# Performance work log

Hardware: AMD Instinct MI355X
Metric: run time of the kernel (lower is better)

Reference implementation:

```python
import jax, jax.numpy as jnp
import numpy as np

N = 50000
E = 800000
IN_CH = 256
OUT_CH = 64   # per-head channels (PyG out_channels)
HEADS = 4
NEG_SLOPE = 0.2


def setup_inputs() -> dict:
    key = jax.random.key(0)
    k = jax.random.split(key, 8)
    x = jax.random.normal(k[0], (N, IN_CH), dtype=jnp.float32)
    edge_index = jax.random.randint(k[1], (2, E), 0, N, dtype=jnp.int64)
    # GATConv parameters
    W = jax.random.normal(k[2], (IN_CH, HEADS * OUT_CH), dtype=jnp.float32) * (1.0 / np.sqrt(IN_CH))
    att_src = jax.random.normal(k[3], (HEADS, OUT_CH), dtype=jnp.float32) * 0.1
    att_dst = jax.random.normal(k[4], (HEADS, OUT_CH), dtype=jnp.float32) * 0.1
    bias = jnp.zeros((OUT_CH,), dtype=jnp.float32)
    # residual linear (bias=False)
    W_res = jax.random.normal(k[5], (IN_CH, OUT_CH), dtype=jnp.float32) * (1.0 / np.sqrt(IN_CH))
    return {"x": x, "edge_index": edge_index, "W": W, "att_src": att_src,
            "att_dst": att_dst, "bias": bias, "W_res": W_res}


def _gat_forward(x, edge_index, W, att_src, att_dst, bias, W_res):
    # residual branch
    x_res = x @ W_res                                   # [N, OUT_CH]

    # node transform: [N, H, C]
    xw = (x @ W).reshape(N, HEADS, OUT_CH)
    # per-node attention logits, [N, H]
    a_src = jnp.einsum('nhc,hc->nh', xw, att_src)
    a_dst = jnp.einsum('nhc,hc->nh', xw, att_dst)

    # add self-loops (PyG GATConv default add_self_loops=True)
    loops = jnp.arange(N, dtype=edge_index.dtype)
    src = jnp.concatenate([edge_index[0], loops])       # [E+N]
    dst = jnp.concatenate([edge_index[1], loops])       # [E+N]

    # per-edge logits + leaky relu, [E+N, H]
    alpha = jax.nn.leaky_relu(a_src[src] + a_dst[dst], NEG_SLOPE)

    # segment softmax over destination nodes
    m = jax.ops.segment_max(alpha, dst, num_segments=N)    # [N, H]
    e = jnp.exp(alpha - m[dst])
    denom = jax.ops.segment_sum(e, dst, num_segments=N)    # [N, H]
    a = e / denom[dst]                                     # [E+N, H]
    # (dropout p=0.1 on attention coeffs is identity in eval mode)

    # weighted scatter-aggregate: [N, H, C]
    msgs = xw[src] * a[:, :, None]
    out = jax.ops.segment_sum(msgs, dst, num_segments=N)

    # concat=False -> mean over heads, then bias
    x_conv = out.mean(axis=1) + bias                     # [N, OUT_CH]
    return jax.nn.relu(x_conv + x_res)


def reference(x, edge_index, W, att_src, att_dst, bias, W_res):
    return _gat_forward(x, edge_index, W, att_src, att_dst, bias, W_res)
```

## Files before the change

### kernel.cpp

```cpp
#include <hip/hip_runtime.h>
#include <math.h>

#define N_NODES 50000
#define N_EDGES 800000
#define IN_CH   256
#define OUT_CH  64
#define HEADS   4
#define NEG_SLOPE 0.2f
#define NCOLS   320
#define NTILES  20
#define NKK     8
#define PACK_BLOCKS 40
#define GEMM_BLOCKS 782
#define SCAN_BLOCKS 196
#define HIST_BLOCKS 3125
#define SCAT_BLOCKS 3125
#define AGG_BLOCKS  6250

typedef __attribute__((ext_vector_type(8))) short short8;
typedef __attribute__((ext_vector_type(4))) float f32x4;

__device__ __forceinline__ float lrelu(float v) {
    return v > 0.f ? v : NEG_SLOPE * v;
}
__device__ __forceinline__ unsigned bf16_rne(float f) {
    unsigned u = __float_as_uint(f);
    return (u + 0x7FFFu + ((u >> 16) & 1u)) >> 16;
}
__device__ __forceinline__ unsigned pack2(float lo, float hi) {
    return bf16_rne(lo) | (bf16_rne(hi) << 16);
}
__device__ __forceinline__ float bflo(unsigned u) { return __uint_as_float(u << 16); }
__device__ __forceinline__ float bfhi(unsigned u) { return __uint_as_float(u & 0xFFFF0000u); }
__device__ __forceinline__ short8 as_short8(uint4 u) {
    union { uint4 u4; short8 s8; } cv; cv.u4 = u; return cv.s8;
}

__global__ __launch_bounds__(256) void pack_B(
    const float* __restrict__ W, const float* __restrict__ Wres,
    uint4* __restrict__ Bp)
{
    const int idx  = blockIdx.x * 256 + threadIdx.x;
    const int kk   = idx / (NTILES * 64);
    const int rem  = idx - kk * (NTILES * 64);
    const int t    = rem >> 6;
    const int lane = rem & 63;
    const int colL = lane & 15, quad = lane >> 4;
    const int col  = t * 16 + colL;
    const int k0   = kk * 32 + quad * 8;
    float v[8];
    #pragma unroll
    for (int j = 0; j < 8; ++j) {
        const int k = k0 + j;
        v[j] = (col < IN_CH) ? W[(size_t)k * IN_CH + col]
                             : Wres[(size_t)k * OUT_CH + (col - IN_CH)];
    }
    uint4 u;
    u.x = pack2(v[0], v[1]); u.y = pack2(v[2], v[3]);
    u.z = pack2(v[4], v[5]); u.w = pack2(v[6], v[7]);
    Bp[(kk * NTILES + t) * 64 + lane] = u;
}

__global__ __launch_bounds__(256) void hist_gemm(
    const float* __restrict__ x, const uint4* __restrict__ Bp,
    uint2* __restrict__ xw2, float* __restrict__ xres,
    const int* __restrict__ ei, int* __restrict__ cnt,
    int* __restrict__ epos,
    const float* __restrict__ attS, const float* __restrict__ attD,
    float* __restrict__ asrc, float* __restrict__ adst)
{
    __shared__ uint4 Alds[4 * NKK * 64];
    __shared__ float logS[64][HEADS];
    __shared__ float logD[64][HEADS];

    if (blockIdx.x >= GEMM_BLOCKS) {
        const int e = (blockIdx.x - GEMM_BLOCKS) * 256 + threadIdx.x;
        if (e < N_EDGES)
            epos[e] = atomicAdd(&cnt[ei[N_EDGES + e]], 1);
        return;
    }

    const int tid = threadIdx.x;
    const int n0  = blockIdx.x * 64;

    logS[tid >> 2][tid & 3] = 0.f;
    logD[tid >> 2][tid & 3] = 0.f;

    #pragma unroll
    for (int i = 0; i < 8; ++i) {
        const int e    = i * 256 + tid;
        const int g    = e >> 9;
        const int kk   = (e >> 6) & 7;
        const int lane = e & 63;
        const int cL   = lane & 15, qd = lane >> 4;
        const int row  = n0 + g * 16 + cL;
        const int k0   = kk * 32 + qd * 8;
        uint4 u = make_uint4(0u, 0u, 0u, 0u);
        if (row < N_NODES) {
            const float4 a = *reinterpret_cast<const float4*>(x + (size_t)row * IN_CH + k0);
            const float4 b = *reinterpret_cast<const float4*>(x + (size_t)row * IN_CH + k0 + 4);
            u.x = pack2(a.x, a.y); u.y = pack2(a.z, a.w);
            u.z = pack2(b.x, b.y); u.w = pack2(b.z, b.w);
        }
        Alds[(g * NKK + kk) * 64 + lane] = u;
    }
    __syncthreads();

    const int lane = tid & 63;
    const int wv   = tid >> 6;
    const int colL = lane & 15, quad = lane >> 4;

    f32x4 acc[4][5];
    #pragma unroll
    for (int rg = 0; rg < 4; ++rg)
        #pragma unroll
        for (int j = 0; j < 5; ++j) acc[rg][j] = (f32x4){0.f, 0.f, 0.f, 0.f};

    for (int kk = 0; kk < NKK; ++kk) {
        uint4 bu[5];
        #pragma unroll
        for (int j = 0; j < 5; ++j)
            bu[j] = Bp[(kk * NTILES + j * 4 + wv) * 64 + lane];
        #pragma unroll
        for (int rg = 0; rg < 4; ++rg) {
            const short8 a = as_short8(Alds[(rg * NKK + kk) * 64 + lane]);
            #pragma unroll
            for (int j = 0; j < 5; ++j)
                acc[rg][j] = __builtin_amdgcn_mfma_f32_16x16x32_bf16(
                    a, as_short8(bu[j]), acc[rg][j], 0, 0, 0);
        }
    }

    #pragma unroll
    for (int rg = 0; rg < 4; ++rg) {
        #pragma unroll
        for (int r = 0; r < 4; ++r) {
            const int row = n0 + rg * 16 + quad * 4 + r;
            if (row < N_NODES) {
                xw2[(size_t)row * 64 + wv * 16 + colL] = make_uint2(
                    pack2(acc[rg][0][r], acc[rg][1][r]),
                    pack2(acc[rg][2][r], acc[rg][3][r]));
                xres[(size_t)row * OUT_CH + wv * 16 + colL] = acc[rg][4][r];
            }
        }
    }

    float aSr[HEADS], aDr[HEADS];
    #pragma unroll
    for (int h = 0; h < HEADS; ++h) {
        aSr[h] = attS[h * 64 + wv * 16 + colL];
        aDr[h] = attD[h * 64 + wv * 16 + colL];
    }
    #pragma unroll
    for (int rg = 0; rg < 4; ++rg) {
        #pragma unroll
        for (int h = 0; h < HEADS; ++h) {
            #pragma unroll
            for (int r = 0; r < 4; ++r) {
                float vS = acc[rg][h][r] * aSr[h];
                float vD = acc[rg][h][r] * aDr[h];
                #pragma unroll
                for (int m = 1; m < 16; m <<= 1) {
                    vS += __shfl_xor(vS, m);
                    vD += __shfl_xor(vD, m);
                }
                if (colL == 0) {
                    atomicAdd(&logS[rg * 16 + quad * 4 + r][h], vS);
                    atomicAdd(&logD[rg * 16 + quad * 4 + r][h], vD);
                }
            }
        }
    }
    __syncthreads();
    {
        const int rl = tid >> 2, h = tid & 3;
        const int row = n0 + rl;
        if (row < N_NODES) {
            asrc[(size_t)row * HEADS + h] = logS[rl][h];
            adst[(size_t)row * HEADS + h] = logD[rl][h];
        }
    }
}

__global__ __launch_bounds__(256) void scan_local(
    const int* __restrict__ cnt, int* __restrict__ lscan, int* __restrict__ bsum)
{
    __shared__ int ws[4];
    const int t = threadIdx.x, lane = t & 63, w = t >> 6;
    const int i = blockIdx.x * 256 + t;
    const int v = (i < N_NODES) ? cnt[i] : 0;
    int sc = v;
    #pragma unroll
    for (int off = 1; off < 64; off <<= 1) {
        const int n = __shfl_up(sc, off);
        if (lane >= off) sc += n;
    }
    if (lane == 63) ws[w] = sc;
    __syncthreads();
    int prefix = 0;
    for (int j = 0; j < w; ++j) prefix += ws[j];
    if (i < N_NODES) lscan[i] = prefix + sc - v;
    if (t == 255) bsum[blockIdx.x] = prefix + sc;
}

__global__ __launch_bounds__(256) void scatter_edges(
    const int* __restrict__ ei, const int* __restrict__ epos,
    const int* __restrict__ lscan, const int* __restrict__ bsum,
    int* __restrict__ esrc)
{
    __shared__ int bsx[256];
    __shared__ int ws[4];
    const int t = threadIdx.x;
    const int lane = t & 63, wv = t >> 6;

    const int v = (t < SCAN_BLOCKS) ? bsum[t] : 0;
    int sc = v;
    #pragma unroll
    for (int off = 1; off < 64; off <<= 1) {
        const int n = __shfl_up(sc, off);
        if (lane >= off) sc += n;
    }
    if (lane == 63) ws[wv] = sc;
    __syncthreads();
    int prefix = 0;
    for (int j = 0; j < wv; ++j) prefix += ws[j];
    bsx[t] = prefix + sc - v;
    __syncthreads();

    const int e = blockIdx.x * 256 + t;
    if (e < N_EDGES) {
        const int d = ei[N_EDGES + e];
        esrc[lscan[d] + bsx[d >> 8] + epos[e]] = ei[e];
    }
}

__global__ __launch_bounds__(256) void aggregate(
    const int* __restrict__ esrc, const int* __restrict__ lscan,
    const int* __restrict__ bsum, const int* __restrict__ cnt,
    const float* __restrict__ asrc, const float* __restrict__ adst,
    const uint2* __restrict__ xw2, const float* __restrict__ xres,
    const float* __restrict__ bias, float* __restrict__ out,
    const int d0)
{
    __shared__ float4 wbuf[4][64];
    __shared__ int    sbuf[4][64];
    __shared__ int    bsx[256];
    __shared__ int    ws[4];
    const int t = threadIdx.x;
    const int lane = t & 63;
    const int wv   = t >> 6;

    {
        const int v = (t < SCAN_BLOCKS) ? bsum[t] : 0;
        int sc = v;
        #pragma unroll
        for (int off = 1; off < 64; off <<= 1) {
            const int n = __shfl_up(sc, off);
            if (lane >= off) sc += n;
        }
        if (lane == 63) ws[wv] = sc;
        __syncthreads();
        int prefix = 0;
        for (int j = 0; j < wv; ++j) prefix += ws[j];
        bsx[t] = prefix + sc - v;
        __syncthreads();
    }

    const int d = d0 + blockIdx.x * 4 + wv;
    const int row = lscan[d] + bsx[d >> 8];
    const int deg = cnt[d];
    const float4 ad = *reinterpret_cast<const float4*>(adst + (size_t)d * 4);
    const char* xwB = (const char*)xw2;
    const int laneB = lane << 3;

    float dn0 = 0.f, dn1 = 0.f, dn2 = 0.f, dn3 = 0.f;
    float ac0 = 0.f, ac1 = 0.f, ac2 = 0.f, ac3 = 0.f;

    for (int base = 0; base < deg; base += 64) {
        const int m = min(64, deg - base);
        if (lane < m) {
            const int s = esrc[row + base + lane];
            const float4 as = *reinterpret_cast<const float4*>(asrc + (size_t)s * 4);
            const float e0 = __expf(lrelu(as.x + ad.x));
            const float e1 = __expf(lrelu(as.y + ad.y));
            const float e2 = __expf(lrelu(as.z + ad.z));
            const float e3 = __expf(lrelu(as.w + ad.w));
            dn0 += e0; dn1 += e1; dn2 += e2; dn3 += e3;
            wbuf[wv][lane] = make_float4(e0, e1, e2, e3);
            sbuf[wv][lane] = s << 9;
        }
        int j = 0;
        for (; j + 4 <= m; j += 4) {
            uint2 v0 = *(const uint2*)(xwB + sbuf[wv][j]     + laneB);
            uint2 v1 = *(const uint2*)(xwB + sbuf[wv][j + 1] + laneB);
            uint2 v2 = *(const uint2*)(xwB + sbuf[wv][j + 2] + laneB);
            uint2 v3 = *(const uint2*)(xwB + sbuf[wv][j + 3] + laneB);
            {
                const float4 w = wbuf[wv][j];
                ac0 = fmaf(w.x, bflo(v0.x), ac0); ac1 = fmaf(w.y, bfhi(v0.x), ac1);
                ac2 = fmaf(w.z, bflo(v0.y), ac2); ac3 = fmaf(w.w, bfhi(v0.y), ac3);
            }
            {
                const float4 w = wbuf[wv][j + 1];
                ac0 = fmaf(w.x, bflo(v1.x), ac0); ac1 = fmaf(w.y, bfhi(v1.x), ac1);
                ac2 = fmaf(w.z, bflo(v1.y), ac2); ac3 = fmaf(w.w, bfhi(v1.y), ac3);
            }
            {
                const float4 w = wbuf[wv][j + 2];
                ac0 = fmaf(w.x, bflo(v2.x), ac0); ac1 = fmaf(w.y, bfhi(v2.x), ac1);
                ac2 = fmaf(w.z, bflo(v2.y), ac2); ac3 = fmaf(w.w, bfhi(v2.y), ac3);
            }
            {
                const float4 w = wbuf[wv][j + 3];
                ac0 = fmaf(w.x, bflo(v3.x), ac0); ac1 = fmaf(w.y, bfhi(v3.x), ac1);
                ac2 = fmaf(w.z, bflo(v3.y), ac2); ac3 = fmaf(w.w, bfhi(v3.y), ac3);
            }
        }
        for (; j < m; ++j) {
            const float4 w = wbuf[wv][j];
            const uint2 v = *(const uint2*)(xwB + sbuf[wv][j] + laneB);
            ac0 = fmaf(w.x, bflo(v.x), ac0);
            ac1 = fmaf(w.y, bfhi(v.x), ac1);
            ac2 = fmaf(w.z, bflo(v.y), ac2);
            ac3 = fmaf(w.w, bfhi(v.y), ac3);
        }
    }

    #pragma unroll
    for (int off = 32; off >= 1; off >>= 1) {
        dn0 += __shfl_xor(dn0, off);
        dn1 += __shfl_xor(dn1, off);
        dn2 += __shfl_xor(dn2, off);
        dn3 += __shfl_xor(dn3, off);
    }
    const float4 asd = *reinterpret_cast<const float4*>(asrc + (size_t)d * 4);
    const float s0 = __expf(lrelu(asd.x + ad.x));
    const float s1 = __expf(lrelu(asd.y + ad.y));
    const float s2 = __expf(lrelu(asd.z + ad.z));
    const float s3 = __expf(lrelu(asd.w + ad.w));
    const uint2 u = xw2[(size_t)d * 64 + lane];
    ac0 = fmaf(s0, bflo(u.x), ac0); ac1 = fmaf(s1, bfhi(u.x), ac1);
    ac2 = fmaf(s2, bflo(u.y), ac2); ac3 = fmaf(s3, bfhi(u.y), ac3);
    const float i0 = 0.25f / (dn0 + s0);
    const float i1 = 0.25f / (dn1 + s1);
    const float i2 = 0.25f / (dn2 + s2);
    const float i3 = 0.25f / (dn3 + s3);
    const float v = ac0 * i0 + ac1 * i1 + ac2 * i2 + ac3 * i3
                  + bias[lane] + xres[(size_t)d * OUT_CH + lane];
    out[(size_t)d * OUT_CH + lane] = fmaxf(v, 0.f);
}

extern "C" void kernel_launch(void* const* d_in, const int* in_sizes, int n_in,
                              void* d_out, int out_size, void* d_ws, size_t ws_size,
                              hipStream_t stream) {
    const float* x    = (const float*)d_in[0];
    const int*   ei   = (const int*)d_in[1];
    const float* W    = (const float*)d_in[2];
    const float* attS = (const float*)d_in[3];
    const float* attD = (const float*)d_in[4];
    const float* bias = (const float*)d_in[5];
    const float* Wres = (const float*)d_in[6];
    float* out = (float*)d_out;

    char* p = (char*)d_ws;
    uint4*    Bp    = (uint4*)p;    p += (size_t)NKK * NTILES * 64 * 16;
    uint2*    xw2   = (uint2*)p;    p += (size_t)N_NODES * 64 * 8;
    float*    xres  = (float*)p;    p += (size_t)N_NODES * OUT_CH * 4;
    float*    asrc  = (float*)p;    p += (size_t)N_NODES * HEADS * 4;
    float*    adst  = (float*)p;    p += (size_t)N_NODES * HEADS * 4;
    int*      cnt   = (int*)p;      p += (size_t)N_NODES * 4;
    int*      lscan = (int*)p;      p += (size_t)N_NODES * 4;
    int*      bsum  = (int*)p;      p += 256 * 4;
    int*      epos  = (int*)p;      p += (size_t)N_EDGES * 4;
    int*      esrc  = (int*)p;      p += (size_t)N_EDGES * 4;

    hipMemsetAsync(cnt, 0, (size_t)N_NODES * sizeof(int), stream);

    pack_B<<<PACK_BLOCKS, 256, 0, stream>>>(W, Wres, Bp);
    hist_gemm<<<GEMM_BLOCKS + HIST_BLOCKS, 256, 0, stream>>>(
        x, Bp, xw2, xres, ei, cnt, epos, attS, attD, asrc, adst);
    scan_local<<<SCAN_BLOCKS, 256, 0, stream>>>(cnt, lscan, bsum);
    scatter_edges<<<SCAT_BLOCKS, 256, 0, stream>>>(
        ei, epos, lscan, bsum, esrc);
    aggregate<<<AGG_BLOCKS, 256, 0, stream>>>(
        esrc, lscan, bsum, cnt, asrc, adst, xw2, xres, bias, out, 0);
    aggregate<<<AGG_BLOCKS, 256, 0, stream>>>(
        esrc, lscan, bsum, cnt, asrc, adst, xw2, xres, bias, out, 25000);
}
```

Baseline: 253.3 us.

## Privatize degree histogram per XCD with workgroup-scope atomics and merge launches

The edge-degree histogram now keeps a separate counter array for each XCD, chosen from the hardware XCC_ID register. Atomics use workgroup memory scope instead of device scope, meant to avoid cross-die coherence traffic on the counter array. The scan folds the per-XCD counts into per-node bases, and the scatter adds the XCD base so each edge gets a unique slot. The two aggregate launches are merged into one. This trades 8x more counter memory, extra memset and scan work for cheaper atomics. It relies on workgroup-scope atomics being correct across CUs of one XCD sharing L2.

```diff
diff --git a/kernel.cpp b/kernel.cpp
--- a/kernel.cpp
+++ b/kernel.cpp
@@ -10,12 +10,13 @@
 #define NCOLS   320
 #define NTILES  20
 #define NKK     8
+#define NXCD    8
 #define PACK_BLOCKS 40
 #define GEMM_BLOCKS 782
 #define SCAN_BLOCKS 196
 #define HIST_BLOCKS 3125
 #define SCAT_BLOCKS 3125
-#define AGG_BLOCKS  6250
+#define AGG_BLOCKS  12500
 
 typedef __attribute__((ext_vector_type(8))) short short8;
 typedef __attribute__((ext_vector_type(4))) float f32x4;
@@ -64,7 +65,7 @@
 __global__ __launch_bounds__(256) void hist_gemm(
     const float* __restrict__ x, const uint4* __restrict__ Bp,
     uint2* __restrict__ xw2, float* __restrict__ xres,
-    const int* __restrict__ ei, int* __restrict__ cnt,
+    const int* __restrict__ ei, int* __restrict__ cnt8,
     int* __restrict__ epos,
     const float* __restrict__ attS, const float* __restrict__ attD,
     float* __restrict__ asrc, float* __restrict__ adst)
@@ -75,8 +76,16 @@
 
     if (blockIdx.x >= GEMM_BLOCKS) {
         const int e = (blockIdx.x - GEMM_BLOCKS) * 256 + threadIdx.x;
-        if (e < N_EDGES)
-            epos[e] = atomicAdd(&cnt[ei[N_EDGES + e]], 1);
+        if (e < N_EDGES) {
+            int xcc;
+            asm volatile("s_getreg_b32 %0, hwreg(HW_REG_XCC_ID)" : "=s"(xcc));
+            xcc &= 7;
+            const int d = ei[N_EDGES + e];
+            const int pos = __hip_atomic_fetch_add(
+                &cnt8[(size_t)xcc * N_NODES + d], 1,
+                __ATOMIC_RELAXED, __HIP_MEMORY_SCOPE_WORKGROUP);
+            epos[e] = (xcc << 24) | pos;
+        }
         return;
     }
 
@@ -183,12 +192,23 @@
 }
 
 __global__ __launch_bounds__(256) void scan_local(
-    const int* __restrict__ cnt, int* __restrict__ lscan, int* __restrict__ bsum)
+    const int* __restrict__ cnt8, int* __restrict__ ctot,
+    int* __restrict__ xbase, int* __restrict__ lscan, int* __restrict__ bsum)
 {
     __shared__ int ws[4];
     const int t = threadIdx.x, lane = t & 63, w = t >> 6;
     const int i = blockIdx.x * 256 + t;
-    const int v = (i < N_NODES) ? cnt[i] : 0;
+    int v = 0;
+    if (i < N_NODES) {
+        int run = 0;
+        #pragma unroll
+        for (int xc = 0; xc < NXCD; ++xc) {
+            xbase[(size_t)xc * N_NODES + i] = run;
+            run += cnt8[(size_t)xc * N_NODES + i];
+        }
+        v = run;
+        ctot[i] = v;
+    }
     int sc = v;
     #pragma unroll
     for (int off = 1; off < 64; off <<= 1) {
@@ -206,7 +226,7 @@
 __global__ __launch_bounds__(256) void scatter_edges(
     const int* __restrict__ ei, const int* __restrict__ epos,
     const int* __restrict__ lscan, const int* __restrict__ bsum,
-    int* __restrict__ esrc)
+    const int* __restrict__ xbase, int* __restrict__ esrc)
 {
     __shared__ int bsx[256];
     __shared__ int ws[4];
@@ -230,17 +250,19 @@
     const int e = blockIdx.x * 256 + t;
     if (e < N_EDGES) {
         const int d = ei[N_EDGES + e];
-        esrc[lscan[d] + bsx[d >> 8] + epos[e]] = ei[e];
+        const int p = epos[e];
+        const int xc = p >> 24;
+        esrc[lscan[d] + bsx[d >> 8] + xbase[(size_t)xc * N_NODES + d]
+             + (p & 0xFFFFFF)] = ei[e];
     }
 }
 
 __global__ __launch_bounds__(256) void aggregate(
     const int* __restrict__ esrc, const int* __restrict__ lscan,
-    const int* __restrict__ bsum, const int* __restrict__ cnt,
+    const int* __restrict__ bsum, const int* __restrict__ ctot,
     const float* __restrict__ asrc, const float* __restrict__ adst,
     const uint2* __restrict__ xw2, const float* __restrict__ xres,
-    const float* __restrict__ bias, float* __restrict__ out,
-    const int d0)
+    const float* __restrict__ bias, float* __restrict__ out)
 {
     __shared__ float4 wbuf[4][64];
     __shared__ int    sbuf[4][64];
@@ -266,9 +288,9 @@
         __syncthreads();
     }
 
-    const int d = d0 + blockIdx.x * 4 + wv;
+    const int d = blockIdx.x * 4 + wv;
     const int row = lscan[d] + bsx[d >> 8];
-    const int deg = cnt[d];
+    const int deg = ctot[d];
     const float4 ad = *reinterpret_cast<const float4*>(adst + (size_t)d * 4);
     const char* xwB = (const char*)xw2;
     const int laneB = lane << 3;
@@ -368,22 +390,22 @@
     float*    xres  = (float*)p;    p += (size_t)N_NODES * OUT_CH * 4;
     float*    asrc  = (float*)p;    p += (size_t)N_NODES * HEADS * 4;
     float*    adst  = (float*)p;    p += (size_t)N_NODES * HEADS * 4;
-    int*      cnt   = (int*)p;      p += (size_t)N_NODES * 4;
+    int*      cnt8  = (int*)p;      p += (size_t)NXCD * N_NODES * 4;
+    int*      ctot  = (int*)p;      p += (size_t)N_NODES * 4;
+    int*      xbase = (int*)p;      p += (size_t)NXCD * N_NODES * 4;
     int*      lscan = (int*)p;      p += (size_t)N_NODES * 4;
     int*      bsum  = (int*)p;      p += 256 * 4;
     int*      epos  = (int*)p;      p += (size_t)N_EDGES * 4;
     int*      esrc  = (int*)p;      p += (size_t)N_EDGES * 4;
 
-    hipMemsetAsync(cnt, 0, (size_t)N_NODES * sizeof(int), stream);
+    hipMemsetAsync(cnt8, 0, (size_t)NXCD * N_NODES * sizeof(int), stream);
 
     pack_B<<<PACK_BLOCKS, 256, 0, stream>>>(W, Wres, Bp);
     hist_gemm<<<GEMM_BLOCKS + HIST_BLOCKS, 256, 0, stream>>>(
-        x, Bp, xw2, xres, ei, cnt, epos, attS, attD, asrc, adst);
-    scan_local<<<SCAN_BLOCKS, 256, 0, stream>>>(cnt, lscan, bsum);
+        x, Bp, xw2, xres, ei, cnt8, epos, attS, attD, asrc, adst);
+    scan_local<<<SCAN_BLOCKS, 256, 0, stream>>>(cnt8, ctot, xbase, lscan, bsum);
     scatter_edges<<<SCAT_BLOCKS, 256, 0, stream>>>(
-        ei, epos, lscan, bsum, esrc);
+        ei, epos, lscan, bsum, xbase, esrc);
     aggregate<<<AGG_BLOCKS, 256, 0, stream>>>(
-        esrc, lscan, bsum, cnt, asrc, adst, xw2, xres, bias, out, 0);
-    aggregate<<<AGG_BLOCKS, 256, 0, stream>>>(
-        esrc, lscan, bsum, cnt, asrc, adst, xw2, xres, bias, out, 25000);
-}
+        esrc, lscan, bsum, ctot, asrc, adst, xw2, xres, bias, out);
+}
```

Result: faster. 242.8 us (-4.1%).

## Replace global atomic CSR build with two-level binned radix partition

Applied to the files above, without the earlier changes.

Replaces the per-edge global atomic histogram and random scatter with a two-pass binned partition. Edges are first counted into 391 coarse bins of 128 destinations using LDS histograms per block, then partitioned into a packed mid buffer, then counted and scattered within each bin using shared-memory atomics. This is meant to remove contended global atomics and the epos array, and to make the scatter writes local. The two aggregate launches are also merged into one. In exchange it adds several small kernel launches, and the 17-bit packing of source indices only holds while N stays below 131072.

```diff
diff --git a/kernel.cpp b/kernel.cpp
--- a/kernel.cpp
+++ b/kernel.cpp
@@ -13,9 +13,10 @@
 #define PACK_BLOCKS 40
 #define GEMM_BLOCKS 782
 #define SCAN_BLOCKS 196
-#define HIST_BLOCKS 3125
-#define SCAT_BLOCKS 3125
-#define AGG_BLOCKS  6250
+#define NBINS   391
+#define P1_BLOCKS 256
+#define EPB     3125
+#define AGG_BLOCKS 12500
 
 typedef __attribute__((ext_vector_type(8))) short short8;
 typedef __attribute__((ext_vector_type(4))) float f32x4;
@@ -61,11 +62,10 @@
     Bp[(kk * NTILES + t) * 64 + lane] = u;
 }
 
-__global__ __launch_bounds__(256) void hist_gemm(
+__global__ __launch_bounds__(256) void gemm_hist(
     const float* __restrict__ x, const uint4* __restrict__ Bp,
     uint2* __restrict__ xw2, float* __restrict__ xres,
-    const int* __restrict__ ei, int* __restrict__ cnt,
-    int* __restrict__ epos,
+    const int* __restrict__ ei, int* __restrict__ M,
     const float* __restrict__ attS, const float* __restrict__ attD,
     float* __restrict__ asrc, float* __restrict__ adst)
 {
@@ -74,9 +74,20 @@
     __shared__ float logD[64][HEADS];
 
     if (blockIdx.x >= GEMM_BLOCKS) {
-        const int e = (blockIdx.x - GEMM_BLOCKS) * 256 + threadIdx.x;
-        if (e < N_EDGES)
-            epos[e] = atomicAdd(&cnt[ei[N_EDGES + e]], 1);
+        const int blk = blockIdx.x - GEMM_BLOCKS;
+        int* lh = (int*)Alds;
+        for (int b = threadIdx.x; b < NBINS; b += 256) lh[b] = 0;
+        __syncthreads();
+        const int e0 = blk * EPB;
+        #pragma unroll
+        for (int r = 0; r < 13; ++r) {
+            const int idx = (r << 8) + threadIdx.x;
+            if (idx < EPB)
+                atomicAdd(&lh[ei[N_EDGES + e0 + idx] >> 7], 1);
+        }
+        __syncthreads();
+        for (int b = threadIdx.x; b < NBINS; b += 256)
+            M[(size_t)b * P1_BLOCKS + blk] = lh[b];
         return;
     }
 
@@ -182,6 +193,90 @@
     }
 }
 
+__global__ __launch_bounds__(256) void binscan_M(
+    int* __restrict__ M, int* __restrict__ binCnt)
+{
+    __shared__ int ws[4];
+    const int t = threadIdx.x, lane = t & 63, w = t >> 6;
+    const int b = blockIdx.x;
+    const int v = M[(size_t)b * P1_BLOCKS + t];
+    int sc = v;
+    #pragma unroll
+    for (int off = 1; off < 64; off <<= 1) {
+        const int n = __shfl_up(sc, off);
+        if (lane >= off) sc += n;
+    }
+    if (lane == 63) ws[w] = sc;
+    __syncthreads();
+    int prefix = 0;
+    for (int j = 0; j < w; ++j) prefix += ws[j];
+    M[(size_t)b * P1_BLOCKS + t] = prefix + sc - v;
+    if (t == 255) binCnt[b] = prefix + sc;
+}
+
+__global__ __launch_bounds__(512) void binstart_scan(
+    const int* __restrict__ binCnt, int* __restrict__ binStart)
+{
+    __shared__ int ws[8];
+    const int t = threadIdx.x, lane = t & 63, w = t >> 6;
+    const int v = (t < NBINS) ? binCnt[t] : 0;
+    int sc = v;
+    #pragma unroll
+    for (int off = 1; off < 64; off <<= 1) {
+        const int n = __shfl_up(sc, off);
+        if (lane >= off) sc += n;
+    }
+    if (lane == 63) ws[w] = sc;
+    __syncthreads();
+    int prefix = 0;
+    for (int j = 0; j < w; ++j) prefix += ws[j];
+    if (t < NBINS) binStart[t] = prefix + sc - v;
+}
+
+__global__ __launch_bounds__(256) void part_mid(
+    const int* __restrict__ ei, const int* __restrict__ M,
+    const int* __restrict__ binStart, unsigned* __restrict__ mid)
+{
+    __shared__ int baseL[NBINS];
+    __shared__ int lh[NBINS];
+    const int blk = blockIdx.x;
+    for (int b = threadIdx.x; b < NBINS; b += 256) {
+        baseL[b] = binStart[b] + M[(size_t)b * P1_BLOCKS + blk];
+        lh[b] = 0;
+    }
+    __syncthreads();
+    const int e0 = blk * EPB;
+    #pragma unroll
+    for (int r = 0; r < 13; ++r) {
+        const int idx = (r << 8) + threadIdx.x;
+        if (idx < EPB) {
+            const int e = e0 + idx;
+            const int d = ei[N_EDGES + e];
+            const int b = d >> 7;
+            const int pos = atomicAdd(&lh[b], 1);
+            mid[baseL[b] + pos] = ((unsigned)(d & 127) << 17) | (unsigned)ei[e];
+        }
+    }
+}
+
+__global__ __launch_bounds__(256) void count_fine(
+    const unsigned* __restrict__ mid, const int* __restrict__ binStart,
+    const int* __restrict__ binCnt, int* __restrict__ cnt)
+{
+    __shared__ int c128[128];
+    const int t = threadIdx.x, b = blockIdx.x;
+    if (t < 128) c128[t] = 0;
+    __syncthreads();
+    const int base = binStart[b], n = binCnt[b];
+    for (int i = t; i < n; i += 256)
+        atomicAdd(&c128[mid[base + i] >> 17], 1);
+    __syncthreads();
+    if (t < 128) {
+        const int d = (b << 7) + t;
+        if (d < N_NODES) cnt[d] = c128[t];
+    }
+}
+
 __global__ __launch_bounds__(256) void scan_local(
     const int* __restrict__ cnt, int* __restrict__ lscan, int* __restrict__ bsum)
 {
@@ -203,15 +298,15 @@
     if (t == 255) bsum[blockIdx.x] = prefix + sc;
 }
 
-__global__ __launch_bounds__(256) void scatter_edges(
-    const int* __restrict__ ei, const int* __restrict__ epos,
-    const int* __restrict__ lscan, const int* __restrict__ bsum,
-    int* __restrict__ esrc)
+__global__ __launch_bounds__(256) void scatter_fine(
+    const unsigned* __restrict__ mid, const int* __restrict__ binStart,
+    const int* __restrict__ binCnt, const int* __restrict__ lscan,
+    const int* __restrict__ bsum, int* __restrict__ esrc)
 {
     __shared__ int bsx[256];
     __shared__ int ws[4];
-    const int t = threadIdx.x;
-    const int lane = t & 63, wv = t >> 6;
+    __shared__ int lh[128];
+    const int t = threadIdx.x, lane = t & 63, wv = t >> 6;
 
     const int v = (t < SCAN_BLOCKS) ? bsum[t] : 0;
     int sc = v;
@@ -221,16 +316,22 @@
         if (lane >= off) sc += n;
     }
     if (lane == 63) ws[wv] = sc;
+    if (t < 128) lh[t] = 0;
     __syncthreads();
     int prefix = 0;
     for (int j = 0; j < wv; ++j) prefix += ws[j];
     bsx[t] = prefix + sc - v;
     __syncthreads();
 
-    const int e = blockIdx.x * 256 + t;
-    if (e < N_EDGES) {
-        const int d = ei[N_EDGES + e];
-        esrc[lscan[d] + bsx[d >> 8] + epos[e]] = ei[e];
+    const int b = blockIdx.x;
+    const int base = binStart[b], n = binCnt[b];
+    for (int i = t; i < n; i += 256) {
+        const unsigned m = mid[base + i];
+        const int dlo = (int)(m >> 17);
+        const int src = (int)(m & 0x1FFFFu);
+        const int d = (b << 7) + dlo;
+        const int pos = atomicAdd(&lh[dlo], 1);
+        esrc[lscan[d] + bsx[d >> 8] + pos] = src;
     }
 }
 
@@ -239,8 +340,7 @@
     const int* __restrict__ bsum, const int* __restrict__ cnt,
     const float* __restrict__ asrc, const float* __restrict__ adst,
     const uint2* __restrict__ xw2, const float* __restrict__ xres,
-    const float* __restrict__ bias, float* __restrict__ out,
-    const int d0)
+    const float* __restrict__ bias, float* __restrict__ out)
 {
     __shared__ float4 wbuf[4][64];
     __shared__ int    sbuf[4][64];
@@ -266,7 +366,7 @@
         __syncthreads();
     }
 
-    const int d = d0 + blockIdx.x * 4 + wv;
+    const int d = blockIdx.x * 4 + wv;
     const int row = lscan[d] + bsx[d >> 8];
     const int deg = cnt[d];
     const float4 ad = *reinterpret_cast<const float4*>(adst + (size_t)d * 4);
@@ -363,27 +463,29 @@
     float* out = (float*)d_out;
 
     char* p = (char*)d_ws;
-    uint4*    Bp    = (uint4*)p;    p += (size_t)NKK * NTILES * 64 * 16;
-    uint2*    xw2   = (uint2*)p;    p += (size_t)N_NODES * 64 * 8;
-    float*    xres  = (float*)p;    p += (size_t)N_NODES * OUT_CH * 4;
-    float*    asrc  = (float*)p;    p += (size_t)N_NODES * HEADS * 4;
-    float*    adst  = (float*)p;    p += (size_t)N_NODES * HEADS * 4;
-    int*      cnt   = (int*)p;      p += (size_t)N_NODES * 4;
-    int*      lscan = (int*)p;      p += (size_t)N_NODES * 4;
-    int*      bsum  = (int*)p;      p += 256 * 4;
-    int*      epos  = (int*)p;      p += (size_t)N_EDGES * 4;
-    int*      esrc  = (int*)p;      p += (size_t)N_EDGES * 4;
-
-    hipMemsetAsync(cnt, 0, (size_t)N_NODES * sizeof(int), stream);
+    uint4*    Bp      = (uint4*)p;    p += (size_t)NKK * NTILES * 64 * 16;
+    uint2*    xw2     = (uint2*)p;    p += (size_t)N_NODES * 64 * 8;
+    float*    xres    = (float*)p;    p += (size_t)N_NODES * OUT_CH * 4;
+    float*    asrc    = (float*)p;    p += (size_t)N_NODES * HEADS * 4;
+    float*    adst    = (float*)p;    p += (size_t)N_NODES * HEADS * 4;
+    int*      M       = (int*)p;      p += (size_t)NBINS * P1_BLOCKS * 4;
+    int*      binCnt  = (int*)p;      p += 512 * 4;
+    int*      binStart= (int*)p;      p += 512 * 4;
+    int*      cnt     = (int*)p;      p += (size_t)N_NODES * 4;
+    int*      lscan   = (int*)p;      p += (size_t)N_NODES * 4;
+    int*      bsum    = (int*)p;      p += 256 * 4;
+    unsigned* mid     = (unsigned*)p; p += (size_t)N_EDGES * 4;
+    int*      esrc    = (int*)p;      p += (size_t)N_EDGES * 4;
 
     pack_B<<<PACK_BLOCKS, 256, 0, stream>>>(W, Wres, Bp);
-    hist_gemm<<<GEMM_BLOCKS + HIST_BLOCKS, 256, 0, stream>>>(
-        x, Bp, xw2, xres, ei, cnt, epos, attS, attD, asrc, adst);
+    gemm_hist<<<GEMM_BLOCKS + P1_BLOCKS, 256, 0, stream>>>(
+        x, Bp, xw2, xres, ei, M, attS, attD, asrc, adst);
+    binscan_M<<<NBINS, 256, 0, stream>>>(M, binCnt);
+    binstart_scan<<<1, 512, 0, stream>>>(binCnt, binStart);
+    part_mid<<<P1_BLOCKS, 256, 0, stream>>>(ei, M, binStart, mid);
+    count_fine<<<NBINS, 256, 0, stream>>>(mid, binStart, binCnt, cnt);
     scan_local<<<SCAN_BLOCKS, 256, 0, stream>>>(cnt, lscan, bsum);
-    scatter_edges<<<SCAT_BLOCKS, 256, 0, stream>>>(
-        ei, epos, lscan, bsum, esrc);
+    scatter_fine<<<NBINS, 256, 0, stream>>>(mid, binStart, binCnt, lscan, bsum, esrc);
     aggregate<<<AGG_BLOCKS, 256, 0, stream>>>(
-        esrc, lscan, bsum, cnt, asrc, adst, xw2, xres, bias, out, 0);
-    aggregate<<<AGG_BLOCKS, 256, 0, stream>>>(
-        esrc, lscan, bsum, cnt, asrc, adst, xw2, xres, bias, out, 25000);
-}
+        esrc, lscan, bsum, cnt, asrc, adst, xw2, xres, bias, out);
+}
```

Result: faster. 241.0 us (-4.8%).
